# Kernel tuning notes

Measured on AMD Instinct MI355X. Metric: run time of the kernel, lower is better.

Reference implementation:

```python
import jax, jax.numpy as jnp
import numpy as np

K = 2          # diffusion steps
HID = 64       # hidden_dim
T_OUT = 12     # decoder horizon
EPS = 1e-6


def _random_walk(A):
    # W_fwd = D_out^{-1} A ; W_bwd = D_in^{-1} A^T  (row-normalized)
    W_fwd = A / (A.sum(axis=1, keepdims=True) + EPS)
    AT = A.T
    W_bwd = AT / (AT.sum(axis=1, keepdims=True) + EPS)
    return W_fwd, W_bwd


def _dconv(xin, Wf, Wb, W, b):
    # xin: (B, N, F). K forward + K backward random-walk hops, concat, linear.
    outs = [xin]
    xf = xin
    for _ in range(K):
        xf = jnp.einsum('ij,bjf->bif', Wf, xf)
        outs.append(xf)
    xb = xin
    for _ in range(K):
        xb = jnp.einsum('ij,bjf->bif', Wb, xb)
        outs.append(xb)
    return jnp.concatenate(outs, axis=-1) @ W + b


def _cell(xl, h, Wr, br, Wz, bz, Wn, bn, Wf, Wb):
    xh = jnp.concatenate([xl, h], axis=-1)
    r = jax.nn.sigmoid(_dconv(xh, Wf, Wb, Wr, br))
    z = jax.nn.sigmoid(_dconv(xh, Wf, Wb, Wz, bz))
    xrh = jnp.concatenate([xl, r * h], axis=-1)
    n = jnp.tanh(_dconv(xrh, Wf, Wb, Wn, bn))
    return (1.0 - z) * h + z * n


def setup_inputs() -> dict:
    key = jax.random.key(0)
    ks = jax.random.split(key, 20)
    B, T_in, N = 16, 12, 512
    x = jax.random.normal(ks[0], (B, T_in, N), dtype=jnp.float32)
    A = jax.random.uniform(ks[1], (N, N), dtype=jnp.float32)

    def lin(k, fan_in, fan_out):
        s = 1.0 / np.sqrt(fan_in)
        kw, kb = jax.random.split(k)
        W = jax.random.uniform(kw, (fan_in, fan_out), jnp.float32, -s, s)
        b = jax.random.uniform(kb, (fan_out,), jnp.float32, -s, s)
        return W, b

    in0 = (2 * K + 1) * (1 + HID)    # 325
    in1 = (2 * K + 1) * (2 * HID)    # 640
    Wr0, br0 = lin(ks[2], in0, HID)
    Wz0, bz0 = lin(ks[3], in0, HID)
    Wn0, bn0 = lin(ks[4], in0, HID)
    Wr1, br1 = lin(ks[5], in1, HID)
    Wz1, bz1 = lin(ks[6], in1, HID)
    Wn1, bn1 = lin(ks[7], in1, HID)
    Wp, bp = lin(ks[8], HID, 1)
    return dict(x=x, A=A, Wr0=Wr0, br0=br0, Wz0=Wz0, bz0=bz0, Wn0=Wn0, bn0=bn0,
                Wr1=Wr1, br1=br1, Wz1=Wz1, bz1=bz1, Wn1=Wn1, bn1=bn1, Wp=Wp, bp=bp)


def reference(x, A, Wr0, br0, Wz0, bz0, Wn0, bn0,
              Wr1, br1, Wz1, bz1, Wn1, bn1, Wp, bp):
    Wf, Wb = _random_walk(A)
    B, T_in, N = x.shape
    x4 = x[..., None]                             # (B, T_in, N, 1)
    h0 = jnp.zeros((B, N, HID), x.dtype)
    h1 = jnp.zeros((B, N, HID), x.dtype)

    def enc_step(carry, xt):
        h0, h1 = carry
        h0 = _cell(xt, h0, Wr0, br0, Wz0, bz0, Wn0, bn0, Wf, Wb)
        h1 = _cell(h0, h1, Wr1, br1, Wz1, bz1, Wn1, bn1, Wf, Wb)
        return (h0, h1), None

    (h0, h1), _ = jax.lax.scan(enc_step, (h0, h1), jnp.moveaxis(x4, 1, 0))

    def dec_step(carry, _):
        h0, h1, di = carry
        h0 = _cell(di, h0, Wr0, br0, Wz0, bz0, Wn0, bn0, Wf, Wb)
        h1 = _cell(h0, h1, Wr1, br1, Wz1, bz1, Wn1, bn1, Wf, Wb)
        yt = h1 @ Wp + bp                          # (B, N, 1)
        return (h0, h1, yt), yt

    (_, _, _), ys = jax.lax.scan(dec_step, (h0, h1, x4[:, -1]), None, length=T_OUT)
    return jnp.moveaxis(ys, 0, 1)[..., 0]          # (B, T_out, N)
```

## Files before the change

### kernel.cpp

```cpp
#include <hip/hip_runtime.h>
#include <math.h>

#define T_IN   12
#define T_OUT  12
#define NB     8192
#define EPSV   1e-6f

typedef __attribute__((ext_vector_type(8))) short short8;
typedef __attribute__((ext_vector_type(4))) float floatx4;

__device__ __forceinline__ unsigned short f2bf(float x) {
    union { float f; unsigned u; } v; v.f = x;
    unsigned r = v.u + 0x7fffu + ((v.u >> 16) & 1u);
    return (unsigned short)(r >> 16);
}
__device__ __forceinline__ float bf2f(unsigned short h) {
    union { float f; unsigned u; } v; v.u = ((unsigned)h) << 16;
    return v.f;
}
__device__ __forceinline__ unsigned packbf(float v) {
    unsigned u = __float_as_uint(v);
    unsigned hu = u & 0xffff0000u;
    float r = v - __uint_as_float(hu);
    unsigned ru = __float_as_uint(r);
    return (ru & 0xffff0000u) | (u >> 16);
}
__device__ __forceinline__ void split2(float v, short& h, short& l) {
    unsigned u = __float_as_uint(v);
    h = (short)(u >> 16);
    float r = v - __uint_as_float(u & 0xffff0000u);
    l = (short)(__float_as_uint(r) >> 16);
}

__device__ __forceinline__ float sigmoid_fast(float x) {
    return 1.0f / (1.0f + __expf(-x));
}
__device__ __forceinline__ float tanh_fast(float x) {
    float e = __expf(2.0f * x);
    return 1.0f - 2.0f / (e + 1.0f);
}

struct HopA {
    const float* M[4];
    float* dst0[4];
};

struct HopM {
    const unsigned short* Ahi[4]; const unsigned short* Alo[4];
    const unsigned* src0; const unsigned* src1;
    unsigned* dst0[4]; unsigned* dst1[4];
    int tiles0;
};

struct XHopM {
    const unsigned short* Ahi[4]; const unsigned short* Alo[4];
    const float* X;
    float* Y;
    int ncols;
};

struct WPack { const float* w[4]; unsigned short* hi[4]; unsigned short* lo[4]; };

struct LPackAll { const float* W[6]; unsigned short* hi[6]; unsigned short* lo[6]; };

struct LinJob {
    const unsigned* seg[10]; int nseg;
    const float* sx[5]; int sxrow[5]; int nsx;
    const unsigned short* Wh[2]; const unsigned short* Wl[2];
    const float* WO[2]; const float* bias[2];
    const float* h; unsigned* GP; float* Z;
};

struct NJob {
    const unsigned* seg[10]; int nseg; int ksplit;
    const float* sx[5]; int sxrow[5]; int nsx;
    const unsigned short* Wh; const unsigned short* Wl;
    const float* WO; const float* bias;
    const float* Zb; const float* hin; float* hout; unsigned* hPout;
    int doProj; const float* Wp; const float* bp; float* out; float* di; int t;
};

__global__ void sumfill_kernel(const float* __restrict__ A, float* __restrict__ Wf,
                               float* __restrict__ Wb) {
    int i = blockIdx.x;
    int t = threadIdx.x;
    __shared__ float s1[256], s2[256];
    float a = A[i * 512 + t] + A[i * 512 + t + 256];
    float b = A[t * 512 + i] + A[(t + 256) * 512 + i];
    s1[t] = a; s2[t] = b;
    __syncthreads();
    for (int off = 128; off > 0; off >>= 1) {
        if (t < off) { s1[t] += s1[t + off]; s2[t] += s2[t + off]; }
        __syncthreads();
    }
    float irs = 1.0f / (s1[0] + EPSV);
    float ics = 1.0f / (s2[0] + EPSV);
    for (int j = t; j < 512; j += 256) {
        Wf[i * 512 + j] = A[i * 512 + j] * irs;
        Wb[i * 512 + j] = A[j * 512 + i] * ics;
    }
}

__global__ void xenc_kernel(const float* __restrict__ x, float* __restrict__ xenc) {
    int idx = blockIdx.x * 256 + threadIdx.x;
    if (idx >= T_IN * NB) return;
    int j = idx & 511;
    int b = (idx >> 9) & 15;
    int t = idx >> 13;
    xenc[t * NB + j * 16 + b] = x[(b * T_IN + t) * 512 + j];
}

__global__ __launch_bounds__(256) void ghop_kernel(HopA a) {
    int z = blockIdx.z;
    const float* Wm = a.M[z];
    const float* X = Wm;
    float* Y = a.dst0[z];
    int col0 = blockIdx.x * 64;
    int row0 = blockIdx.y * 64;
    int tid = threadIdx.x;
    int tx = tid & 15, ty = tid >> 4;
    int kkA = tid & 15, rrA = tid >> 4;
    int ccB = tid & 63, kkB = tid >> 6;

    __shared__ float As[16][68], Bs[16][68];
    float acc[4][4] = {};

    const float* wp = Wm + (row0 + rrA) * 512 + kkA;
    const float* xp = X + (size_t)(col0 + ccB) + (size_t)kkB * 512;

    float ra[4], rb[4];
#pragma unroll
    for (int p = 0; p < 4; ++p) ra[p] = wp[p * 16 * 512];
#pragma unroll
    for (int p = 0; p < 4; ++p) rb[p] = xp[(size_t)(p * 4) * 512];

    for (int k0 = 0; k0 < 512; k0 += 16) {
#pragma unroll
        for (int p = 0; p < 4; ++p) As[kkA][rrA + p * 16] = ra[p];
#pragma unroll
        for (int p = 0; p < 4; ++p) Bs[kkB + p * 4][ccB] = rb[p];
        __syncthreads();
        if (k0 + 16 < 512) {
            int kn = k0 + 16;
#pragma unroll
            for (int p = 0; p < 4; ++p) ra[p] = wp[p * 16 * 512 + kn];
#pragma unroll
            for (int p = 0; p < 4; ++p) rb[p] = xp[(size_t)(kn + p * 4) * 512];
        }
#pragma unroll
        for (int k = 0; k < 16; ++k) {
            const float4 a4 = *(const float4*)&As[k][ty * 4];
            const float4 b4 = *(const float4*)&Bs[k][tx * 4];
            float av[4] = { a4.x, a4.y, a4.z, a4.w };
            float bv[4] = { b4.x, b4.y, b4.z, b4.w };
#pragma unroll
            for (int i = 0; i < 4; ++i)
#pragma unroll
                for (int j = 0; j < 4; ++j)
                    acc[i][j] = fmaf(av[i], bv[j], acc[i][j]);
        }
        __syncthreads();
    }

    int colw = col0 + tx * 4;
#pragma unroll
    for (int i = 0; i < 4; ++i) {
        int row = row0 + ty * 4 + i;
        *(float4*)&Y[(size_t)row * 512 + colw] =
            make_float4(acc[i][0], acc[i][1], acc[i][2], acc[i][3]);
    }
}

__global__ void wpack_kernel(WPack a) {
    int z = blockIdx.y;
    int idx = blockIdx.x * 256 + threadIdx.x;
    int m = idx >> 9, k = idx & 511;
    float x = a.w[z][idx];
    unsigned short h = f2bf(x);
    unsigned short l = f2bf(x - bf2f(h));
    int p = (((m >> 4) * 64 + (k >> 3)) * 16 + (m & 15)) * 8 + (k & 7);
    a.hi[z][p] = h;
    a.lo[z][p] = l;
}

__global__ void lpack_all_kernel(LPackAll p) {
    int g = blockIdx.y;
    int nseg = (g < 3) ? 5 : 10;
    int idx = blockIdx.x * 256 + threadIdx.x;
    if (idx >= nseg * 4096) return;
    int j = idx & 7, ln = (idx >> 3) & 15, ntl = (idx >> 7) & 3, O = idx >> 9;
    int s = O >> 3, o8 = O & 7;
    int base = (g < 3) ? (65 * s + 1) : (64 * s);
    int row = base + o8 * 8 + j;
    int col = ntl * 16 + ln;
    float v = p.W[g][(size_t)row * 64 + col];
    unsigned short h = f2bf(v);
    p.hi[g][idx] = h;
    p.lo[g][idx] = f2bf(v - bf2f(h));
}

template<int MI>
__global__ __launch_bounds__(256) void hop_mfma(HopM a) {
    int z = blockIdx.z;
    int nt = blockIdx.x;
    const unsigned* X; unsigned* Y; int c0;
    if (nt < a.tiles0) { X = a.src0; Y = a.dst0[z]; c0 = nt * 64; }
    else { X = a.src1; Y = a.dst1[z]; c0 = (nt - a.tiles0) * 64; }
    const unsigned short* Ahi = a.Ahi[z];
    const unsigned short* Alo = a.Alo[z];
    int bm = blockIdx.y * (MI * 32);

    __shared__ unsigned short Bhi_s[2][64][40];
    __shared__ unsigned short Blo_s[2][64][40];

    int tid = threadIdx.x;
    int lane = tid & 63, w = tid >> 6;
    int wm = (w & 1) * (MI * 16), wn = (w >> 1) * 32;
    int ln = lane & 15, quad = lane >> 4;
    int sc = tid & 63, skh = tid >> 6;

    floatx4 acc[MI][2];
#pragma unroll
    for (int mi = 0; mi < MI; ++mi)
#pragma unroll
        for (int ci = 0; ci < 2; ++ci) acc[mi][ci] = (floatx4)0.0f;

    const unsigned* xbase = X + c0 + sc;
    int mtb = (bm + wm) >> 4;

    unsigned uv[8];
#pragma unroll
    for (int j = 0; j < 8; ++j)
        uv[j] = xbase[(size_t)(skh * 8 + j) * 1024];
    {
        short8 h8, l8;
#pragma unroll
        for (int j = 0; j < 8; ++j) {
            h8[j] = (short)(uv[j] & 0xffffu);
            l8[j] = (short)(uv[j] >> 16);
        }
        *(short8*)&Bhi_s[0][sc][skh * 8] = h8;
        *(short8*)&Blo_s[0][sc][skh * 8] = l8;
    }
#pragma unroll
    for (int j = 0; j < 8; ++j)
        uv[j] = xbase[(size_t)(32 + skh * 8 + j) * 1024];

    for (int it = 0; it < 16; ++it) {
        __syncthreads();
        int cur = it & 1;
        if (it + 1 < 16) {
            short8 h8, l8;
#pragma unroll
            for (int j = 0; j < 8; ++j) {
                h8[j] = (short)(uv[j] & 0xffffu);
                l8[j] = (short)(uv[j] >> 16);
            }
            *(short8*)&Bhi_s[cur ^ 1][sc][skh * 8] = h8;
            *(short8*)&Blo_s[cur ^ 1][sc][skh * 8] = l8;
        }
        if (it + 2 < 16) {
            int kn = (it + 2) * 32;
#pragma unroll
            for (int j = 0; j < 8; ++j)
                uv[j] = xbase[(size_t)(kn + skh * 8 + j) * 1024];
        }
        short8 bh[2], bl[2];
#pragma unroll
        for (int ci = 0; ci < 2; ++ci) {
            bh[ci] = *(const short8*)&Bhi_s[cur][wn + ci * 16 + ln][quad * 8];
            bl[ci] = *(const short8*)&Blo_s[cur][wn + ci * 16 + ln][quad * 8];
        }
        int kob = it * 4 + quad;
#pragma unroll
        for (int mi = 0; mi < MI; ++mi) {
            size_t aoff = ((size_t)((mtb + mi) * 64 + kob) * 16 + ln) * 8;
            short8 Ah = *(const short8*)(Ahi + aoff);
            short8 Al = *(const short8*)(Alo + aoff);
#pragma unroll
            for (int ci = 0; ci < 2; ++ci) {
                acc[mi][ci] = __builtin_amdgcn_mfma_f32_16x16x32_bf16(Ah, bh[ci], acc[mi][ci], 0, 0, 0);
                acc[mi][ci] = __builtin_amdgcn_mfma_f32_16x16x32_bf16(Ah, bl[ci], acc[mi][ci], 0, 0, 0);
                acc[mi][ci] = __builtin_amdgcn_mfma_f32_16x16x32_bf16(Al, bh[ci], acc[mi][ci], 0, 0, 0);
            }
        }
    }

#pragma unroll
    for (int mi = 0; mi < MI; ++mi) {
#pragma unroll
        for (int ci = 0; ci < 2; ++ci) {
            int mrow = bm + wm + mi * 16 + quad * 4;
            int col = c0 + wn + ci * 16 + ln;
#pragma unroll
            for (int r = 0; r < 4; ++r)
                Y[(size_t)(mrow + r) * 1024 + col] = packbf(acc[mi][ci][r]);
        }
    }
}

__global__ __launch_bounds__(256) void xhop_mfma(XHopM a) {
    int z = blockIdx.z;
    int c0 = blockIdx.x * 64;
    const unsigned short* Ahi = a.Ahi[z];
    const unsigned short* Alo = a.Alo[z];
    int bm = blockIdx.y * 64;

    __shared__ unsigned short Bhi_s[2][64][40];
    __shared__ unsigned short Blo_s[2][64][40];

    int tid = threadIdx.x;
    int lane = tid & 63, w = tid >> 6;
    int wm = (w & 1) * 32, wn = (w >> 1) * 32;
    int ln = lane & 15, quad = lane >> 4;
    int sc = tid & 63, skh = tid >> 6;

    floatx4 acc[2][2];
#pragma unroll
    for (int mi = 0; mi < 2; ++mi)
#pragma unroll
        for (int ci = 0; ci < 2; ++ci) acc[mi][ci] = (floatx4)0.0f;

    int colS = c0 + sc;
    bool ok = colS < a.ncols;
    const float* xb = a.X + (size_t)(colS >> 4) * NB + (colS & 15);
    int mtb = (bm + wm) >> 4;

    float xv[8];
#pragma unroll
    for (int j = 0; j < 8; ++j)
        xv[j] = ok ? xb[(size_t)(skh * 8 + j) * 16] : 0.0f;
    {
        short8 h8, l8;
#pragma unroll
        for (int j = 0; j < 8; ++j) { short h, l; split2(xv[j], h, l); h8[j] = h; l8[j] = l; }
        *(short8*)&Bhi_s[0][sc][skh * 8] = h8;
        *(short8*)&Blo_s[0][sc][skh * 8] = l8;
    }
#pragma unroll
    for (int j = 0; j < 8; ++j)
        xv[j] = ok ? xb[(size_t)(32 + skh * 8 + j) * 16] : 0.0f;

    for (int it = 0; it < 16; ++it) {
        __syncthreads();
        int cur = it & 1;
        if (it + 1 < 16) {
            short8 h8, l8;
#pragma unroll
            for (int j = 0; j < 8; ++j) { short h, l; split2(xv[j], h, l); h8[j] = h; l8[j] = l; }
            *(short8*)&Bhi_s[cur ^ 1][sc][skh * 8] = h8;
            *(short8*)&Blo_s[cur ^ 1][sc][skh * 8] = l8;
        }
        if (it + 2 < 16) {
            int kn = (it + 2) * 32;
#pragma unroll
            for (int j = 0; j < 8; ++j)
                xv[j] = ok ? xb[(size_t)(kn + skh * 8 + j) * 16] : 0.0f;
        }
        short8 bh[2], bl[2];
#pragma unroll
        for (int ci = 0; ci < 2; ++ci) {
            bh[ci] = *(const short8*)&Bhi_s[cur][wn + ci * 16 + ln][quad * 8];
            bl[ci] = *(const short8*)&Blo_s[cur][wn + ci * 16 + ln][quad * 8];
        }
        int kob = it * 4 + quad;
#pragma unroll
        for (int mi = 0; mi < 2; ++mi) {
            size_t aoff = ((size_t)((mtb + mi) * 64 + kob) * 16 + ln) * 8;
            short8 Ah = *(const short8*)(Ahi + aoff);
            short8 Al = *(const short8*)(Alo + aoff);
#pragma unroll
            for (int ci = 0; ci < 2; ++ci) {
                acc[mi][ci] = __builtin_amdgcn_mfma_f32_16x16x32_bf16(Ah, bh[ci], acc[mi][ci], 0, 0, 0);
                acc[mi][ci] = __builtin_amdgcn_mfma_f32_16x16x32_bf16(Ah, bl[ci], acc[mi][ci], 0, 0, 0);
                acc[mi][ci] = __builtin_amdgcn_mfma_f32_16x16x32_bf16(Al, bh[ci], acc[mi][ci], 0, 0, 0);
            }
        }
    }

#pragma unroll
    for (int mi = 0; mi < 2; ++mi) {
#pragma unroll
        for (int ci = 0; ci < 2; ++ci) {
            int col = c0 + wn + ci * 16 + ln;
            if (col < a.ncols) {
                int mrow = bm + wm + mi * 16 + quad * 4;
                float* yb = a.Y + (size_t)((col >> 4) * 4 + z) * NB + (col & 15);
#pragma unroll
                for (int r = 0; r < 4; ++r)
                    yb[(size_t)(mrow + r) * 16] = acc[mi][ci][r];
            }
        }
    }
}

__device__ __forceinline__ void lin_core2(const unsigned* const* segs, int nseg, int s0,
        const unsigned short* __restrict__ Bh, const unsigned short* __restrict__ Bl,
        int row0, int ln, int quad, int cihalf, floatx4 acc[2]) {
    for (int s = 0; s < nseg; ++s) {
        const unsigned* ap = segs[s] + (size_t)(row0 + ln) * 64 + quad * 8;
#pragma unroll
        for (int hh = 0; hh < 2; ++hh) {
            unsigned u[8];
            *(uint4*)&u[0] = *(const uint4*)(ap + hh * 32);
            *(uint4*)&u[4] = *(const uint4*)(ap + hh * 32 + 4);
            short8 Ah, Al;
#pragma unroll
            for (int j = 0; j < 8; ++j) {
                Ah[j] = (short)(u[j] & 0xffffu);
                Al[j] = (short)(u[j] >> 16);
            }
            int O = (s0 + s) * 8 + hh * 4 + quad;
#pragma unroll
            for (int ci = 0; ci < 2; ++ci) {
                int c_abs = cihalf * 2 + ci;
                size_t boff = ((size_t)(O * 4 + c_abs) * 16 + ln) * 8;
                short8 B1 = *(const short8*)(Bh + boff);
                short8 B2 = *(const short8*)(Bl + boff);
                acc[ci] = __builtin_amdgcn_mfma_f32_16x16x32_bf16(Ah, B1, acc[ci], 0, 0, 0);
                acc[ci] = __builtin_amdgcn_mfma_f32_16x16x32_bf16(Al, B1, acc[ci], 0, 0, 0);
                acc[ci] = __builtin_amdgcn_mfma_f32_16x16x32_bf16(Ah, B2, acc[ci], 0, 0, 0);
            }
        }
    }
}

__device__ __forceinline__ void lin_scalar2p(const float* const* sx, const int* sxrow,
        int nsx, const float* __restrict__ WO,
        int row0, int ln, int quad, int cihalf, floatx4 acc[2]) {
    for (int t = 0; t < nsx; ++t) {
        const float* wr = WO + (size_t)sxrow[t] * 64;
        const float* sv = sx[t] + row0 + quad * 4;
#pragma unroll
        for (int rr = 0; rr < 4; ++rr) {
            float v = sv[rr];
#pragma unroll
            for (int ci = 0; ci < 2; ++ci)
                acc[ci][rr] = fmaf(v, wr[(cihalf * 2 + ci) * 16 + ln], acc[ci][rr]);
        }
    }
}

__device__ __forceinline__ void rz_body(const LinJob& J, int bx) {
    int w = threadIdx.x >> 6, lane = threadIdx.x & 63;
    int ln = lane & 15, quad = lane >> 4;
    int row0 = bx * 64 + w * 16;
    int gate = blockIdx.y;
    int cihalf = blockIdx.z;
    floatx4 acc[2];
    acc[0] = (floatx4)0.0f; acc[1] = (floatx4)0.0f;
    lin_core2(J.seg, J.nseg, 0, J.Wh[gate], J.Wl[gate], row0, ln, quad, cihalf, acc);
    if (J.nsx) lin_scalar2p(J.sx, J.sxrow, J.nsx, J.WO[gate], row0, ln, quad, cihalf, acc);
    const float* bias = J.bias[gate];
#pragma unroll
    for (int ci = 0; ci < 2; ++ci) {
        int col = (cihalf * 2 + ci) * 16 + ln;
        float bv = bias[col];
#pragma unroll
        for (int rr = 0; rr < 4; ++rr) {
            int row = row0 + quad * 4 + rr;
            size_t idx = (size_t)row * 64 + col;
            float sg = sigmoid_fast(acc[ci][rr] + bv);
            if (gate == 0) J.GP[idx] = packbf(sg * J.h[idx]);
            else J.Z[idx] = sg;
        }
    }
}

__global__ __launch_bounds__(256) void lin_rz2(LinJob j0, LinJob j1, int xsplit) {
    if ((int)blockIdx.x >= xsplit) rz_body(j1, (int)blockIdx.x - xsplit);
    else                           rz_body(j0, (int)blockIdx.x);
}

__device__ __forceinline__ void n_body(const NJob& J, int bx) {
    int w = threadIdx.x >> 6, lane = threadIdx.x & 63;
    int ln = lane & 15, quad = lane >> 4;
    int kh = w & 1, cihalf = w >> 1;
    int row0 = bx * 16;
    __shared__ float part[2][2][16][17];
    __shared__ float pr[2][16];
    floatx4 acc[2];
    acc[0] = (floatx4)0.0f; acc[1] = (floatx4)0.0f;
    if (kh == 0) {
        lin_core2(J.seg, J.ksplit, 0, J.Wh, J.Wl, row0, ln, quad, cihalf, acc);
    } else {
        lin_core2(J.seg + J.ksplit, J.nseg - J.ksplit, J.ksplit, J.Wh, J.Wl,
                  row0, ln, quad, cihalf, acc);
        if (J.nsx) lin_scalar2p(J.sx, J.sxrow, J.nsx, J.WO, row0, ln, quad, cihalf, acc);
#pragma unroll
        for (int ci = 0; ci < 2; ++ci)
#pragma unroll
            for (int rr = 0; rr < 4; ++rr)
                part[cihalf][ci][quad * 4 + rr][ln] = acc[ci][rr];
    }
    __syncthreads();
    float p[4] = {0.0f, 0.0f, 0.0f, 0.0f};
    if (kh == 0) {
#pragma unroll
        for (int ci = 0; ci < 2; ++ci) {
            int col = (cihalf * 2 + ci) * 16 + ln;
            float bv = J.bias[col];
            float wpv = J.doProj ? J.Wp[col] : 0.0f;
#pragma unroll
            for (int rr = 0; rr < 4; ++rr) {
                int row = row0 + quad * 4 + rr;
                size_t idx = (size_t)row * 64 + col;
                float pre = acc[ci][rr] + part[cihalf][ci][quad * 4 + rr][ln] + bv;
                float nn = tanh_fast(pre);
                float z = J.Zb[idx];
                float hv = J.hin[idx];
                float o = (1.0f - z) * hv + z * nn;
                J.hout[idx] = o;
                J.hPout[idx] = packbf(o);
                p[rr] = fmaf(o, wpv, p[rr]);
            }
        }
        if (J.doProj) {
#pragma unroll
            for (int rr = 0; rr < 4; ++rr) {
                p[rr] += __shfl_xor(p[rr], 1, 64);
                p[rr] += __shfl_xor(p[rr], 2, 64);
                p[rr] += __shfl_xor(p[rr], 4, 64);
                p[rr] += __shfl_xor(p[rr], 8, 64);
            }
            if (ln == 0) {
#pragma unroll
                for (int rr = 0; rr < 4; ++rr)
                    pr[cihalf][quad * 4 + rr] = p[rr];
            }
        }
    }
    __syncthreads();
    if (J.doProj && kh == 0 && cihalf == 0 && ln == 0) {
        float bpv = J.bp[0];
#pragma unroll
        for (int rr = 0; rr < 4; ++rr) {
            int qr = quad * 4 + rr;
            int row = row0 + qr;
            float y = pr[0][qr] + pr[1][qr] + bpv;
            int n = row >> 4, b = row & 15;
            J.out[(b * T_OUT + J.t) * 512 + n] = y;
            J.di[row] = y;
        }
    }
}

__global__ __launch_bounds__(256) void lin_n2(NJob j0, NJob j1, int xsplit) {
    if ((int)blockIdx.x >= xsplit) n_body(j1, (int)blockIdx.x - xsplit);
    else                           n_body(j0, (int)blockIdx.x);
}

extern "C" void kernel_launch(void* const* d_in, const int* in_sizes, int n_in,
                              void* d_out, int out_size, void* d_ws, size_t ws_size,
                              hipStream_t stream) {
    (void)in_sizes; (void)n_in; (void)out_size; (void)ws_size;
    const float* x   = (const float*)d_in[0];
    const float* A   = (const float*)d_in[1];
    const float* Wr0 = (const float*)d_in[2];  const float* br0 = (const float*)d_in[3];
    const float* Wz0 = (const float*)d_in[4];  const float* bz0 = (const float*)d_in[5];
    const float* Wn0 = (const float*)d_in[6];  const float* bn0 = (const float*)d_in[7];
    const float* Wr1 = (const float*)d_in[8];  const float* br1 = (const float*)d_in[9];
    const float* Wz1 = (const float*)d_in[10]; const float* bz1 = (const float*)d_in[11];
    const float* Wn1 = (const float*)d_in[12]; const float* bn1 = (const float*)d_in[13];
    const float* Wp  = (const float*)d_in[14]; const float* bp  = (const float*)d_in[15];
    float* out = (float*)d_out;

    float* ws = (float*)d_ws;
    size_t off = 0;
    auto alloc = [&](size_t nf) { float* p = ws + off; off += nf; return p; };
    const size_t NB64 = (size_t)NB * 64;
    float* Wf  = alloc(262144); float* Wb  = alloc(262144);
    float* W2f = alloc(262144); float* W2b = alloc(262144);
    float* xenc = alloc((size_t)T_IN * NB);
    unsigned short* Whi[4]; unsigned short* Wlo[4];
    for (int m = 0; m < 4; ++m) Whi[m] = (unsigned short*)alloc(131072);
    for (int m = 0; m < 4; ++m) Wlo[m] = (unsigned short*)alloc(131072);
    unsigned* HAall = (unsigned*)alloc(4 * NB64);
    unsigned* HBall = (unsigned*)alloc(4 * NB64);
    unsigned* HA[4]; unsigned* HB[4]; unsigned* HG0[4]; unsigned* HG1[4];
    for (int m = 0; m < 4; ++m) HA[m] = HAall + m * NB64;
    for (int m = 0; m < 4; ++m) HB[m] = HBall + m * NB64;
    for (int m = 0; m < 4; ++m) HG0[m] = (unsigned*)alloc(NB64);
    for (int m = 0; m < 4; ++m) HG1[m] = (unsigned*)alloc(NB64);
    unsigned* GP0 = (unsigned*)alloc(NB64);
    unsigned* GP1 = (unsigned*)alloc(NB64);
    float* Z0 = alloc(NB64);
    float* Z1 = alloc(NB64);
    float* h0x[2];  h0x[0] = alloc(NB64);  h0x[1] = alloc(NB64);
    unsigned* h0Px[2];
    h0Px[0] = (unsigned*)alloc(NB64); h0Px[1] = (unsigned*)alloc(NB64);
    float* h1 = alloc(NB64);
    unsigned* h1P = (unsigned*)alloc(NB64);
    float* XHE = alloc((size_t)T_IN * 4 * NB);
    float* HXSdec = alloc(4 * NB);
    float* di = alloc(NB);
    unsigned short* LWh[6]; unsigned short* LWl[6];
    for (int g = 0; g < 3; ++g) { LWh[g] = (unsigned short*)alloc(10240); LWl[g] = (unsigned short*)alloc(10240); }
    for (int g = 3; g < 6; ++g) { LWh[g] = (unsigned short*)alloc(20480); LWl[g] = (unsigned short*)alloc(20480); }

    hipMemsetAsync(h0x[1], 0, NB64 * 4, stream);
    hipMemsetAsync(h0Px[1], 0, NB64 * 4, stream);
    hipMemsetAsync(h1, 0, NB64 * 4, stream);
    hipMemsetAsync(h1P, 0, NB64 * 4, stream);
    hipMemsetAsync(HAall, 0, 4 * NB64 * 4, stream);
    hipMemsetAsync(HBall, 0, 4 * NB64 * 4, stream);

    xenc_kernel<<<dim3((T_IN * NB) / 256), 256, 0, stream>>>(x, xenc);
    sumfill_kernel<<<dim3(512), 256, 0, stream>>>(A, Wf, Wb);
    {
        HopA w2 = {};
        w2.M[0] = Wf; w2.M[1] = Wb;
        w2.dst0[0] = W2f; w2.dst0[1] = W2b;
        ghop_kernel<<<dim3(8, 8, 2), 256, 0, stream>>>(w2);
    }
    {
        WPack p;
        p.w[0] = Wf; p.w[1] = W2f; p.w[2] = Wb; p.w[3] = W2b;
        for (int m = 0; m < 4; ++m) { p.hi[m] = Whi[m]; p.lo[m] = Wlo[m]; }
        wpack_kernel<<<dim3(1024, 4), 256, 0, stream>>>(p);
    }
    {
        LPackAll p;
        const float* WG[6] = { Wr0, Wz0, Wn0, Wr1, Wz1, Wn1 };
        for (int g = 0; g < 6; ++g) { p.W[g] = WG[g]; p.hi[g] = LWh[g]; p.lo[g] = LWl[g]; }
        lpack_all_kernel<<<dim3(160, 6), 256, 0, stream>>>(p);
    }
    {
        XHopM xa = {};
        for (int m = 0; m < 4; ++m) { xa.Ahi[m] = Whi[m]; xa.Alo[m] = Wlo[m]; }
        xa.X = xenc; xa.Y = XHE; xa.ncols = 192;
        xhop_mfma<<<dim3(3, 8, 4), 256, 0, stream>>>(xa);
    }

    auto hopSingle = [&](const unsigned* s0, unsigned* const* d0) {
        HopM a = {};
        for (int m = 0; m < 4; ++m) { a.Ahi[m] = Whi[m]; a.Alo[m] = Wlo[m]; }
        a.src0 = s0; a.tiles0 = 16;
        for (int m = 0; m < 4; ++m) a.dst0[m] = d0[m];
        hop_mfma<1><<<dim3(16, 16, 4), 256, 0, stream>>>(a);
    };
    auto hopDual = [&](const unsigned* s0, unsigned* const* d0,
                       const unsigned* s1, unsigned* const* d1) {
        HopM a = {};
        for (int m = 0; m < 4; ++m) { a.Ahi[m] = Whi[m]; a.Alo[m] = Wlo[m]; }
        a.src0 = s0; a.tiles0 = 16;
        for (int m = 0; m < 4; ++m) a.dst0[m] = d0[m];
        a.src1 = s1;
        for (int m = 0; m < 4; ++m) a.dst1[m] = d1[m];
        hop_mfma<2><<<dim3(32, 8, 4), 256, 0, stream>>>(a);
    };

    auto mkRZ1 = [&](int t) {
        LinJob J = {};
        J.seg[0] = h0Px[t & 1]; J.seg[1] = h1P;
        for (int m = 0; m < 4; ++m) { J.seg[2 + 2 * m] = HA[m]; J.seg[3 + 2 * m] = HB[m]; }
        J.nseg = 10; J.nsx = 0;
        J.Wh[0] = LWh[3]; J.Wl[0] = LWl[3]; J.Wh[1] = LWh[4]; J.Wl[1] = LWl[4];
        J.WO[0] = Wr1; J.WO[1] = Wz1; J.bias[0] = br1; J.bias[1] = bz1;
        J.h = h1; J.GP = GP1; J.Z = Z1;
        return J;
    };
    auto mkRZ0 = [&](int tn, const float* xc, const float* hx) {
        LinJob J = {};
        J.seg[0] = h0Px[(tn - 1) & 1];
        for (int m = 0; m < 4; ++m) J.seg[1 + m] = HA[m];
        J.nseg = 5;
        J.nsx = 5;
        J.sx[0] = xc; J.sxrow[0] = 0;
        for (int m = 0; m < 4; ++m) { J.sx[1 + m] = hx + (size_t)m * NB; J.sxrow[1 + m] = 65 * (m + 1); }
        J.Wh[0] = LWh[0]; J.Wl[0] = LWl[0]; J.Wh[1] = LWh[1]; J.Wl[1] = LWl[1];
        J.WO[0] = Wr0; J.WO[1] = Wz0; J.bias[0] = br0; J.bias[1] = bz0;
        J.h = h0x[(tn - 1) & 1]; J.GP = GP0; J.Z = Z0;
        return J;
    };
    auto mkN1 = [&](int t) {
        NJob J = {};
        J.seg[0] = h0Px[t & 1]; J.seg[1] = GP1;
        for (int m = 0; m < 4; ++m) { J.seg[2 + 2 * m] = HA[m]; J.seg[3 + 2 * m] = HG1[m]; }
        J.nseg = 10; J.ksplit = 5; J.nsx = 0;
        J.Wh = LWh[5]; J.Wl = LWl[5]; J.WO = Wn1; J.bias = bn1;
        J.Zb = Z1; J.hin = h1; J.hout = h1; J.hPout = h1P;
        J.doProj = (t >= T_IN); J.Wp = Wp; J.bp = bp; J.out = out; J.di = di; J.t = t - T_IN;
        return J;
    };
    auto mkN0 = [&](int tn, const float* xc, const float* hx) {
        NJob J = {};
        J.seg[0] = GP0;
        for (int m = 0; m < 4; ++m) J.seg[1 + m] = HG0[m];
        J.nseg = 5; J.ksplit = 3;
        J.nsx = 5;
        J.sx[0] = xc; J.sxrow[0] = 0;
        for (int m = 0; m < 4; ++m) { J.sx[1 + m] = hx + (size_t)m * NB; J.sxrow[1 + m] = 65 * (m + 1); }
        J.Wh = LWh[2]; J.Wl = LWl[2]; J.WO = Wn0; J.bias = bn0;
        J.Zb = Z0; J.hin = h0x[(tn - 1) & 1]; J.hout = h0x[tn & 1]; J.hPout = h0Px[tn & 1];
        J.doProj = 0;
        return J;
    };

    auto rz2one = [&](LinJob a) { lin_rz2<<<dim3(128, 2, 2), 256, 0, stream>>>(a, a, 128); };
    auto rz2two = [&](LinJob a, LinJob b) { lin_rz2<<<dim3(256, 2, 2), 256, 0, stream>>>(a, b, 128); };
    auto n2one = [&](NJob a) { lin_n2<<<dim3(512), 256, 0, stream>>>(a, a, 512); };
    auto n2two = [&](NJob a, NJob b) { lin_n2<<<dim3(1024), 256, 0, stream>>>(a, b, 512); };

    rz2one(mkRZ0(0, xenc, XHE));
    hopSingle(GP0, HG0);
    n2one(mkN0(0, xenc, XHE));
    hopSingle(h0Px[0], HA);

    for (int t = 0; t < T_IN + T_OUT; ++t) {
        int tn = t + 1;
        bool last = (t == T_IN + T_OUT - 1);
        bool decFeed = (tn >= T_IN + 1);
        if (!last && !decFeed) {
            int ts = (tn < T_IN) ? tn : (T_IN - 1);
            const float* xc = xenc + (size_t)ts * NB;
            const float* hx = XHE + (size_t)ts * 4 * NB;
            rz2two(mkRZ1(t), mkRZ0(tn, xc, hx));
            hopDual(GP1, HG1, GP0, HG0);
            n2two(mkN1(t), mkN0(tn, xc, hx));
            hopDual(h0Px[tn & 1], HA, h1P, HB);
        } else if (!last) {
            rz2one(mkRZ1(t));
            hopSingle(GP1, HG1);
            n2one(mkN1(t));
            {
                XHopM xo = {};
                for (int m = 0; m < 4; ++m) { xo.Ahi[m] = Whi[m]; xo.Alo[m] = Wlo[m]; }
                xo.X = di; xo.Y = HXSdec; xo.ncols = 16;
                xhop_mfma<<<dim3(1, 8, 4), 256, 0, stream>>>(xo);
            }
            rz2one(mkRZ0(tn, di, HXSdec));
            hopSingle(GP0, HG0);
            n2one(mkN0(tn, di, HXSdec));
            hopDual(h0Px[tn & 1], HA, h1P, HB);
        } else {
            rz2one(mkRZ1(t));
            hopSingle(GP1, HG1);
            n2one(mkN1(t));
        }
    }
}
```

Baseline: 2.780 ms.

## Split decoder layer-0 RZ gates into early partial GEMM plus small finish kernel

```diff
diff --git a/kernel.cpp b/kernel.cpp
--- a/kernel.cpp
+++ b/kernel.cpp
@@ -69,6 +69,8 @@
     const unsigned short* Wh[2]; const unsigned short* Wl[2];
     const float* WO[2]; const float* bias[2];
     const float* h; unsigned* GP; float* Z;
+    float* PR;
+    int mode;
 };
 
 struct NJob {
@@ -78,6 +80,15 @@
     const float* WO; const float* bias;
     const float* Zb; const float* hin; float* hout; unsigned* hPout;
     int doProj; const float* Wp; const float* bp; float* out; float* di; int t;
+};
+
+struct F0 {
+    const float* M[4];
+    const float* di;
+    const float* PR;
+    const float* WO[2]; const float* bias[2];
+    const float* h0;
+    unsigned* GP0; float* Z0; float* HXS;
 };
 
 __global__ void sumfill_kernel(const float* __restrict__ A, float* __restrict__ Wf,
@@ -451,18 +462,31 @@
     acc[0] = (floatx4)0.0f; acc[1] = (floatx4)0.0f;
     lin_core2(J.seg, J.nseg, 0, J.Wh[gate], J.Wl[gate], row0, ln, quad, cihalf, acc);
     if (J.nsx) lin_scalar2p(J.sx, J.sxrow, J.nsx, J.WO[gate], row0, ln, quad, cihalf, acc);
-    const float* bias = J.bias[gate];
-#pragma unroll
-    for (int ci = 0; ci < 2; ++ci) {
-        int col = (cihalf * 2 + ci) * 16 + ln;
-        float bv = bias[col];
-#pragma unroll
-        for (int rr = 0; rr < 4; ++rr) {
-            int row = row0 + quad * 4 + rr;
-            size_t idx = (size_t)row * 64 + col;
-            float sg = sigmoid_fast(acc[ci][rr] + bv);
-            if (gate == 0) J.GP[idx] = packbf(sg * J.h[idx]);
-            else J.Z[idx] = sg;
+    if (J.mode == 0) {
+        const float* bias = J.bias[gate];
+#pragma unroll
+        for (int ci = 0; ci < 2; ++ci) {
+            int col = (cihalf * 2 + ci) * 16 + ln;
+            float bv = bias[col];
+#pragma unroll
+            for (int rr = 0; rr < 4; ++rr) {
+                int row = row0 + quad * 4 + rr;
+                size_t idx = (size_t)row * 64 + col;
+                float sg = sigmoid_fast(acc[ci][rr] + bv);
+                if (gate == 0) J.GP[idx] = packbf(sg * J.h[idx]);
+                else J.Z[idx] = sg;
+            }
+        }
+    } else {
+        float* PRg = J.PR + (size_t)gate * ((size_t)NB * 64);
+#pragma unroll
+        for (int ci = 0; ci < 2; ++ci) {
+            int col = (cihalf * 2 + ci) * 16 + ln;
+#pragma unroll
+            for (int rr = 0; rr < 4; ++rr) {
+                int row = row0 + quad * 4 + rr;
+                PRg[(size_t)row * 64 + col] = acc[ci][rr];
+            }
         }
     }
 }
@@ -550,6 +574,60 @@
     else                           n_body(j0, (int)blockIdx.x);
 }
 
+__global__ __launch_bounds__(256) void finish0_kernel(F0 a) {
+    int n = blockIdx.x;
+    int tid = threadIdx.x;
+    __shared__ float hopS[4][16];
+    __shared__ float sdi[16];
+
+    int g = tid >> 2;
+    int sub = tid & 3;
+    int m = g >> 4, b = g & 15;
+    const float* wrow = a.M[m] + (size_t)n * 512 + sub * 128;
+    const float* dv = a.di + (size_t)(sub * 128) * 16 + b;
+    float s0 = 0.0f, s1 = 0.0f, s2 = 0.0f, s3 = 0.0f;
+#pragma unroll 8
+    for (int k = 0; k < 128; k += 4) {
+        float4 w4 = *(const float4*)&wrow[k];
+        s0 = fmaf(w4.x, dv[(k + 0) * 16], s0);
+        s1 = fmaf(w4.y, dv[(k + 1) * 16], s1);
+        s2 = fmaf(w4.z, dv[(k + 2) * 16], s2);
+        s3 = fmaf(w4.w, dv[(k + 3) * 16], s3);
+    }
+    float sv = (s0 + s1) + (s2 + s3);
+    sv += __shfl_xor(sv, 1, 64);
+    sv += __shfl_xor(sv, 2, 64);
+    if (sub == 0) {
+        hopS[m][b] = sv;
+        a.HXS[(size_t)m * NB + n * 16 + b] = sv;
+    }
+    if (tid < 16) sdi[tid] = a.di[n * 16 + tid];
+    __syncthreads();
+
+    int gate = tid >> 7, col = tid & 63, rh = (tid >> 6) & 1;
+    const float* WOg = a.WO[gate];
+    float w0c = WOg[col];
+    float wmc[4];
+#pragma unroll
+    for (int mm = 0; mm < 4; ++mm)
+        wmc[mm] = WOg[(size_t)(65 * (mm + 1)) * 64 + col];
+    float bv = a.bias[gate][col];
+    const float* PRg = a.PR + (size_t)gate * ((size_t)NB * 64);
+#pragma unroll
+    for (int rr = 0; rr < 8; ++rr) {
+        int bl = rh * 8 + rr;
+        int row = n * 16 + bl;
+        size_t idx = (size_t)row * 64 + col;
+        float pre = PRg[idx] + bv + sdi[bl] * w0c;
+#pragma unroll
+        for (int mm = 0; mm < 4; ++mm)
+            pre = fmaf(hopS[mm][bl], wmc[mm], pre);
+        float sg = sigmoid_fast(pre);
+        if (gate == 0) a.GP0[idx] = packbf(sg * a.h0[idx]);
+        else a.Z0[idx] = sg;
+    }
+}
+
 extern "C" void kernel_launch(void* const* d_in, const int* in_sizes, int n_in,
                               void* d_out, int out_size, void* d_ws, size_t ws_size,
                               hipStream_t stream) {
@@ -575,8 +653,14 @@
     unsigned short* Whi[4]; unsigned short* Wlo[4];
     for (int m = 0; m < 4; ++m) Whi[m] = (unsigned short*)alloc(131072);
     for (int m = 0; m < 4; ++m) Wlo[m] = (unsigned short*)alloc(131072);
-    unsigned* HAall = (unsigned*)alloc(4 * NB64);
-    unsigned* HBall = (unsigned*)alloc(4 * NB64);
+    float* zbase = alloc(12 * NB64);
+    float* h0x[2]; unsigned* h0Px[2];
+    h0x[1]  = zbase;
+    h0Px[1] = (unsigned*)(zbase + NB64);
+    float* h1 = zbase + 2 * NB64;
+    unsigned* h1P = (unsigned*)(zbase + 3 * NB64);
+    unsigned* HAall = (unsigned*)(zbase + 4 * NB64);
+    unsigned* HBall = (unsigned*)(zbase + 8 * NB64);
     unsigned* HA[4]; unsigned* HB[4]; unsigned* HG0[4]; unsigned* HG1[4];
     for (int m = 0; m < 4; ++m) HA[m] = HAall + m * NB64;
     for (int m = 0; m < 4; ++m) HB[m] = HBall + m * NB64;
@@ -586,11 +670,9 @@
     unsigned* GP1 = (unsigned*)alloc(NB64);
     float* Z0 = alloc(NB64);
     float* Z1 = alloc(NB64);
-    float* h0x[2];  h0x[0] = alloc(NB64);  h0x[1] = alloc(NB64);
-    unsigned* h0Px[2];
-    h0Px[0] = (unsigned*)alloc(NB64); h0Px[1] = (unsigned*)alloc(NB64);
-    float* h1 = alloc(NB64);
-    unsigned* h1P = (unsigned*)alloc(NB64);
+    h0x[0]  = alloc(NB64);
+    h0Px[0] = (unsigned*)alloc(NB64);
+    float* PR0 = alloc(2 * NB64);
     float* XHE = alloc((size_t)T_IN * 4 * NB);
     float* HXSdec = alloc(4 * NB);
     float* di = alloc(NB);
@@ -598,12 +680,7 @@
     for (int g = 0; g < 3; ++g) { LWh[g] = (unsigned short*)alloc(10240); LWl[g] = (unsigned short*)alloc(10240); }
     for (int g = 3; g < 6; ++g) { LWh[g] = (unsigned short*)alloc(20480); LWl[g] = (unsigned short*)alloc(20480); }
 
-    hipMemsetAsync(h0x[1], 0, NB64 * 4, stream);
-    hipMemsetAsync(h0Px[1], 0, NB64 * 4, stream);
-    hipMemsetAsync(h1, 0, NB64 * 4, stream);
-    hipMemsetAsync(h1P, 0, NB64 * 4, stream);
-    hipMemsetAsync(HAall, 0, 4 * NB64 * 4, stream);
-    hipMemsetAsync(HBall, 0, 4 * NB64 * 4, stream);
+    hipMemsetAsync(zbase, 0, 12 * NB64 * 4, stream);
 
     xenc_kernel<<<dim3((T_IN * NB) / 256), 256, 0, stream>>>(x, xenc);
     sumfill_kernel<<<dim3(512), 256, 0, stream>>>(A, Wf, Wb);
@@ -657,20 +734,22 @@
         J.nseg = 10; J.nsx = 0;
         J.Wh[0] = LWh[3]; J.Wl[0] = LWl[3]; J.Wh[1] = LWh[4]; J.Wl[1] = LWl[4];
         J.WO[0] = Wr1; J.WO[1] = Wz1; J.bias[0] = br1; J.bias[1] = bz1;
-        J.h = h1; J.GP = GP1; J.Z = Z1;
+        J.h = h1; J.GP = GP1; J.Z = Z1; J.mode = 0;
         return J;
     };
-    auto mkRZ0 = [&](int tn, const float* xc, const float* hx) {
+    auto mkRZ0 = [&](int tn, const float* xc, const float* hx, int mode) {
         LinJob J = {};
         J.seg[0] = h0Px[(tn - 1) & 1];
         for (int m = 0; m < 4; ++m) J.seg[1 + m] = HA[m];
         J.nseg = 5;
-        J.nsx = 5;
-        J.sx[0] = xc; J.sxrow[0] = 0;
-        for (int m = 0; m < 4; ++m) { J.sx[1 + m] = hx + (size_t)m * NB; J.sxrow[1 + m] = 65 * (m + 1); }
+        if (mode == 0) {
+            J.nsx = 5;
+            J.sx[0] = xc; J.sxrow[0] = 0;
+            for (int m = 0; m < 4; ++m) { J.sx[1 + m] = hx + (size_t)m * NB; J.sxrow[1 + m] = 65 * (m + 1); }
+        }
         J.Wh[0] = LWh[0]; J.Wl[0] = LWl[0]; J.Wh[1] = LWh[1]; J.Wl[1] = LWl[1];
         J.WO[0] = Wr0; J.WO[1] = Wz0; J.bias[0] = br0; J.bias[1] = bz0;
-        J.h = h0x[(tn - 1) & 1]; J.GP = GP0; J.Z = Z0;
+        J.h = h0x[(tn - 1) & 1]; J.GP = GP0; J.Z = Z0; J.PR = PR0; J.mode = mode;
         return J;
     };
     auto mkN1 = [&](int t) {
@@ -702,7 +781,7 @@
     auto n2one = [&](NJob a) { lin_n2<<<dim3(512), 256, 0, stream>>>(a, a, 512); };
     auto n2two = [&](NJob a, NJob b) { lin_n2<<<dim3(1024), 256, 0, stream>>>(a, b, 512); };
 
-    rz2one(mkRZ0(0, xenc, XHE));
+    rz2one(mkRZ0(0, xenc, XHE, 0));
     hopSingle(GP0, HG0);
     n2one(mkN0(0, xenc, XHE));
     hopSingle(h0Px[0], HA);
@@ -715,21 +794,23 @@
             int ts = (tn < T_IN) ? tn : (T_IN - 1);
             const float* xc = xenc + (size_t)ts * NB;
             const float* hx = XHE + (size_t)ts * 4 * NB;
-            rz2two(mkRZ1(t), mkRZ0(tn, xc, hx));
+            rz2two(mkRZ1(t), mkRZ0(tn, xc, hx, 0));
             hopDual(GP1, HG1, GP0, HG0);
             n2two(mkN1(t), mkN0(tn, xc, hx));
             hopDual(h0Px[tn & 1], HA, h1P, HB);
         } else if (!last) {
-            rz2one(mkRZ1(t));
+            rz2two(mkRZ1(t), mkRZ0(tn, nullptr, nullptr, 1));
             hopSingle(GP1, HG1);
             n2one(mkN1(t));
             {
-                XHopM xo = {};
-                for (int m = 0; m < 4; ++m) { xo.Ahi[m] = Whi[m]; xo.Alo[m] = Wlo[m]; }
-                xo.X = di; xo.Y = HXSdec; xo.ncols = 16;
-                xhop_mfma<<<dim3(1, 8, 4), 256, 0, stream>>>(xo);
-            }
-            rz2one(mkRZ0(tn, di, HXSdec));
+                F0 f = {};
+                f.M[0] = Wf; f.M[1] = W2f; f.M[2] = Wb; f.M[3] = W2b;
+                f.di = di; f.PR = PR0;
+                f.WO[0] = Wr0; f.WO[1] = Wz0; f.bias[0] = br0; f.bias[1] = bz0;
+                f.h0 = h0x[t & 1];
+                f.GP0 = GP0; f.Z0 = Z0; f.HXS = HXSdec;
+                finish0_kernel<<<dim3(512), 256, 0, stream>>>(f);
+            }
             hopSingle(GP0, HG0);
             n2one(mkN0(tn, di, HXSdec));
             hopDual(h0Px[tn & 1], HA, h1P, HB);
```

After: 2.712 ms. -2.5%, faster.
